# Kernel optimization log

Hardware: AMD Instinct MI355X
Metric: run time of the kernel (lower is better)

Reference implementation:

```python
import jax, jax.numpy as jnp
import numpy as np

H = 4096
N_HEADS = 32
N_KV = 8
HEAD_DIM = H // N_HEADS  # 128
GROUPS = N_HEADS // N_KV  # 4
FFN = 11008
EPS = 1e-5
B = 16
S_CACHE = 4096


def _rms(x, w):
    var = jnp.mean(x * x, axis=-1, keepdims=True)
    return w * (x * jax.lax.rsqrt(var + EPS))


def setup_inputs() -> dict:
    key = jax.random.key(0)
    ks = jax.random.split(key, 12)
    s = 0.02
    return {
        "hidden_states": jax.random.normal(ks[0], (B, 1, H), jnp.float32),
        "k_cache": jax.random.normal(ks[1], (B, N_KV, S_CACHE, HEAD_DIM), jnp.float32),
        "v_cache": jax.random.normal(ks[2], (B, N_KV, S_CACHE, HEAD_DIM), jnp.float32),
        "Wq": jax.random.normal(ks[3], (N_HEADS * HEAD_DIM, H), jnp.float32) * s,
        "Wk": jax.random.normal(ks[4], (N_KV * HEAD_DIM, H), jnp.float32) * s,
        "Wv": jax.random.normal(ks[5], (N_KV * HEAD_DIM, H), jnp.float32) * s,
        "Wo": jax.random.normal(ks[6], (H, N_HEADS * HEAD_DIM), jnp.float32) * s,
        "Wg": jax.random.normal(ks[7], (FFN, H), jnp.float32) * s,
        "Wu": jax.random.normal(ks[8], (FFN, H), jnp.float32) * s,
        "Wd": jax.random.normal(ks[9], (H, FFN), jnp.float32) * s,
        "ln1_w": jnp.ones((H,), jnp.float32),
        "ln2_w": jnp.ones((H,), jnp.float32),
    }


def reference(hidden_states, k_cache, v_cache, Wq, Wk, Wv, Wo, Wg, Wu, Wd, ln1_w, ln2_w):
    b = hidden_states.shape[0]
    residual = hidden_states
    h = _rms(hidden_states, ln1_w)  # [B,1,H]

    q = (h @ Wq.T).reshape(b, N_KV, GROUPS, HEAD_DIM)       # [B,kvH,G,D]
    k_new = (h @ Wk.T).reshape(b, N_KV, 1, HEAD_DIM)         # [B,kvH,1,D]
    v_new = (h @ Wv.T).reshape(b, N_KV, 1, HEAD_DIM)

    k = jnp.concatenate([k_cache, k_new], axis=2)            # [B,kvH,S+1,D]
    v = jnp.concatenate([v_cache, v_new], axis=2)

    scale = 1.0 / np.sqrt(HEAD_DIM)
    # GQA without materializing repeated KV heads (same math as repeat_interleave)
    scores = jnp.einsum("bkgd,bksd->bkgs", q, k) * scale      # [B,kvH,G,S+1]
    probs = jax.nn.softmax(scores.astype(jnp.float32), axis=-1).astype(q.dtype)
    attn = jnp.einsum("bkgs,bksd->bkgd", probs, v)            # [B,kvH,G,D]
    attn = attn.reshape(b, 1, N_HEADS * HEAD_DIM)

    h = residual + attn @ Wo.T                                # [B,1,H]

    residual = h
    h = _rms(h, ln2_w)
    mlp = (jax.nn.silu(h @ Wg.T) * (h @ Wu.T)) @ Wd.T
    return residual + mlp
```

## Files before the change

### kernel.cpp

```cpp
#include <hip/hip_runtime.h>
#include <math.h>

#define HH   4096
#define NKV  8
#define GRP  4
#define HD   128
#define FFN  11008
#define NB   16
#define SC   4096
#define SCALE 0.08838834764831845f
#define SCH  512
#define QKS  8

typedef float f4v __attribute__((ext_vector_type(4)));
typedef float f32x4 __attribute__((ext_vector_type(4)));
typedef short bf16x8 __attribute__((ext_vector_type(8)));
typedef unsigned short u16x4 __attribute__((ext_vector_type(4)));
typedef unsigned int u32x4v __attribute__((ext_vector_type(4)));

__device__ __forceinline__ f4v ntload4(const float* p) {
  return __builtin_nontemporal_load((const f4v*)p);
}
__device__ __forceinline__ float dot4(f4v a, f4v b) {
  return a[0] * b[0] + a[1] * b[1] + a[2] * b[2] + a[3] * b[3];
}
__device__ __forceinline__ unsigned short f2bf(float f) {
  unsigned int u = __builtin_bit_cast(unsigned int, f);
  u += 0x7fffu + ((u >> 16) & 1u);
  return (unsigned short)(u >> 16);
}
__device__ __forceinline__ float silu_f(float g) { return g / (1.f + __expf(-g)); }
__device__ __forceinline__ unsigned int cvtpk(float lo, float hi) {
  unsigned int r;
  asm("v_cvt_pk_bf16_f32 %0, %1, %2" : "=v"(r) : "v"(lo), "v"(hi));
  return r;
}

__global__ void rmsnorm_bf_k(const float* __restrict__ x, const float* __restrict__ w,
                             unsigned short* __restrict__ y) {
  int b = blockIdx.x;
  const float* xb = x + (size_t)b * HH;
  unsigned short* yb = y + (size_t)b * HH;
  int t = threadIdx.x, lane = t & 63, wave = t >> 6;
  f4v v[4];
  float ss = 0.f;
#pragma unroll
  for (int i = 0; i < 4; ++i) {
    v[i] = *(const f4v*)(xb + 4 * (t + 256 * i));
    ss += dot4(v[i], v[i]);
  }
#pragma unroll
  for (int m = 1; m < 64; m <<= 1) ss += __shfl_xor(ss, m);
  __shared__ float red[4];
  if (lane == 0) red[wave] = ss;
  __syncthreads();
  float tot = red[0] + red[1] + red[2] + red[3];
  float rs = rsqrtf(tot * (1.0f / HH) + 1e-5f);
#pragma unroll
  for (int i = 0; i < 4; ++i) {
    int h = 4 * (t + 256 * i);
    f4v wv = *(const f4v*)(w + h);
    f4v o = v[i] * rs * wv;
    u16x4 p;
#pragma unroll
    for (int j = 0; j < 4; ++j) p[j] = f2bf(o[j]);
    *(u16x4*)(yb + h) = p;
  }
}

template <int MODE>
__global__ __launch_bounds__(256, 4) void gemv_mfma_k(
    const float* __restrict__ W0, const float* __restrict__ W1,
    const float* __restrict__ W2, const unsigned short* __restrict__ xbf,
    float* __restrict__ part, int O, int H, int CH) {
  int t = threadIdx.x, lane = t & 63, wave = t >> 6;
  int rb = blockIdx.x, kc = blockIdx.y;
  int obase = rb * 64 + wave * 16;
  int orow = obase + (lane & 15);

  const float* Wp;
  if (MODE == 0) {
    if (orow < 4096) Wp = W0 + (size_t)orow * H;
    else if (orow < 5120) Wp = W1 + (size_t)(orow - 4096) * H;
    else Wp = W2 + (size_t)(orow - 5120) * H;
  } else if (MODE == 2) {
    Wp = (orow < FFN) ? W0 + (size_t)orow * H : W1 + (size_t)(orow - FFN) * H;
  } else {
    Wp = W0 + (size_t)orow * H;
  }

  int k0 = kc * CH + (lane >> 4) * 8;
  const float* wp = Wp + k0;
  const unsigned short* ap = xbf + (size_t)(lane & 15) * H + k0;

  f32x4 acc = {0.f, 0.f, 0.f, 0.f};
  int steps = CH / 32;
#pragma unroll 2
  for (int s = 0; s < steps; ++s) {
    f4v w0 = ntload4(wp);
    f4v w1 = ntload4(wp + 4);
    bf16x8 a = *(const bf16x8*)ap;
    bf16x8 bb;
#pragma unroll
    for (int j = 0; j < 4; ++j) {
      bb[j] = (short)f2bf(w0[j]);
      bb[4 + j] = (short)f2bf(w1[j]);
    }
    acc = __builtin_amdgcn_mfma_f32_16x16x32_bf16(a, bb, acc, 0, 0, 0);
    wp += 32;
    ap += 32;
  }
  float* pb = part + ((size_t)kc * NB + (size_t)((lane >> 4) * 4)) * O + orow;
#pragma unroll
  for (int r = 0; r < 4; ++r) pb[(size_t)r * O] = acc[r];
}

__global__ void rmsnorm2_k(const float* __restrict__ hid, const float* __restrict__ p1,
                           const float* __restrict__ w, float* __restrict__ h2,
                           unsigned short* __restrict__ xn2) {
  int b = blockIdx.x;
  int t = threadIdx.x, lane = t & 63, wave = t >> 6;
  f4v v[4];
  float ss = 0.f;
#pragma unroll
  for (int i = 0; i < 4; ++i) {
    int h = 4 * (t + 256 * i);
    f4v s = *(const f4v*)(hid + (size_t)b * HH + h);
#pragma unroll
    for (int ks = 0; ks < 8; ++ks)
      s += *(const f4v*)(p1 + ((size_t)(ks * NB + b)) * HH + h);
    v[i] = s;
    ss += dot4(s, s);
  }
#pragma unroll
  for (int m = 1; m < 64; m <<= 1) ss += __shfl_xor(ss, m);
  __shared__ float red[4];
  if (lane == 0) red[wave] = ss;
  __syncthreads();
  float tot = red[0] + red[1] + red[2] + red[3];
  float rs = rsqrtf(tot * (1.0f / HH) + 1e-5f);
#pragma unroll
  for (int i = 0; i < 4; ++i) {
    int h = 4 * (t + 256 * i);
    *(f4v*)(h2 + (size_t)b * HH + h) = v[i];
    f4v wv = *(const f4v*)(w + h);
    f4v o = v[i] * rs * wv;
    u16x4 p;
#pragma unroll
    for (int j = 0; j < 4; ++j) p[j] = f2bf(o[j]);
    *(u16x4*)(xn2 + (size_t)b * HH + h) = p;
  }
}

__global__ void red_gu_k(const float* __restrict__ p2, unsigned short* __restrict__ gu) {
  int idx = blockIdx.x * 256 + threadIdx.x;
  int pi = idx % 2752, b = idx / 2752;
  int p = pi * 4;
  const float* g0 = p2 + (size_t)b * 22016 + p;
  f4v g = *(const f4v*)g0 + *(const f4v*)(g0 + (size_t)NB * 22016);
  f4v u = *(const f4v*)(g0 + FFN) + *(const f4v*)(g0 + FFN + (size_t)NB * 22016);
  u16x4 pk;
#pragma unroll
  for (int j = 0; j < 4; ++j) pk[j] = f2bf(silu_f(g[j]) * u[j]);
  *(u16x4*)(gu + (size_t)b * FFN + p) = pk;
}

__global__ void red_out_k(const float* __restrict__ h2, const float* __restrict__ p3,
                          float* __restrict__ out) {
  int idx = blockIdx.x * 256 + threadIdx.x;
  int o = (idx & 1023) * 4, b = idx >> 10;
  f4v s = *(const f4v*)(h2 + (size_t)b * HH + o);
#pragma unroll
  for (int ks = 0; ks < 8; ++ks)
    s += *(const f4v*)(p3 + ((size_t)(ks * NB + b)) * HH + o);
  *(f4v*)(out + (size_t)b * HH + o) = s;
}

__global__ __launch_bounds__(256, 4) void attn_part_k(
    const float* __restrict__ pq, const float* __restrict__ kcache,
    const float* __restrict__ vcache, float* __restrict__ pm,
    float* __restrict__ pl, float* __restrict__ pacc) {
  int c = blockIdx.x, kv = blockIdx.y, b = blockIdx.z;
  int t = threadIdx.x, lane = t & 63, wave = t >> 6;
  int ds = lane & 15, ss = lane >> 4;
  __shared__ float qs[GRP * HD];
  __shared__ float sc[GRP][SCH];
  __shared__ float accw[4][GRP][HD];

  {
    int i0 = t * 2;
#pragma unroll
    for (int i = i0; i < i0 + 2; ++i) {
      int off = kv * (GRP * HD) + i;
      float s = 0.f;
#pragma unroll
      for (int kk = 0; kk < QKS; ++kk)
        s += pq[((size_t)kk * NB + b) * 6144 + off];
      qs[i] = s;
    }
  }
  __syncthreads();

  bf16x8 bq[4];
#pragma unroll
  for (int kk = 0; kk < 4; ++kk) {
    u32x4v w;
#pragma unroll
    for (int jj = 0; jj < 4; ++jj) {
      float f0 = 0.f, f1 = 0.f;
      if (ds < GRP) {
        int d = kk * 32 + ss * 8 + jj * 2;
        f0 = qs[ds * HD + d];
        f1 = qs[ds * HD + d + 1];
      }
      w[jj] = cvtpk(f0, f1);
    }
    bq[kk] = __builtin_bit_cast(bf16x8, w);
  }

  const size_t kvoff = ((size_t)b * NKV + kv) * (size_t)SC * HD;
  const float* kb = kcache + kvoff;

  for (int st = 0; st < SCH / 64; ++st) {
    int prel = (st * 4 + wave) * 16;
    const float* kr = kb + (size_t)(c * SCH + prel + ds) * HD + ss * 8;
    f32x4 d4 = {0.f, 0.f, 0.f, 0.f};
#pragma unroll
    for (int kk = 0; kk < 4; ++kk) {
      f4v k0 = *(const f4v*)(kr + kk * 32);
      f4v k1 = *(const f4v*)(kr + kk * 32 + 4);
      u32x4v w;
      w[0] = cvtpk(k0[0], k0[1]);
      w[1] = cvtpk(k0[2], k0[3]);
      w[2] = cvtpk(k1[0], k1[1]);
      w[3] = cvtpk(k1[2], k1[3]);
      d4 = __builtin_amdgcn_mfma_f32_16x16x32_bf16(
          __builtin_bit_cast(bf16x8, w), bq[kk], d4, 0, 0, 0);
    }
    if (ds < GRP) {
#pragma unroll
      for (int r = 0; r < 4; ++r) sc[ds][prel + ss * 4 + r] = d4[r] * SCALE;
    }
  }
  __syncthreads();

  size_t pbase = (((size_t)(b * NKV + kv)) * 8 + c) * GRP;
  {
    int g = wave;
    float m = -1e30f;
    for (int i = lane; i < SCH; i += 64) m = fmaxf(m, sc[g][i]);
#pragma unroll
    for (int mm = 1; mm < 64; mm <<= 1) m = fmaxf(m, __shfl_xor(m, mm));
    float lsum = 0.f;
    for (int i = lane; i < SCH; i += 64) {
      float e = __expf(sc[g][i] - m);
      sc[g][i] = e;
      lsum += e;
    }
#pragma unroll
    for (int mm = 1; mm < 64; mm <<= 1) lsum += __shfl_xor(lsum, mm);
    if (lane == 0) { pm[pbase + g] = m; pl[pbase + g] = lsum; }
  }
  __syncthreads();

  float acc[GRP][8];
#pragma unroll
  for (int g = 0; g < GRP; ++g)
#pragma unroll
    for (int j = 0; j < 8; ++j) acc[g][j] = 0.f;
  const float* vb = vcache + kvoff;
  for (int st = 0; st < SCH / 16; ++st) {
    int sl = st * 16 + wave * 4 + ss;
    const float* vr = vb + (size_t)(c * SCH + sl) * HD + 8 * ds;
    f4v v0 = ntload4(vr);
    f4v v1 = ntload4(vr + 4);
    float p[GRP];
#pragma unroll
    for (int g = 0; g < GRP; ++g) p[g] = sc[g][sl];
#pragma unroll
    for (int g = 0; g < GRP; ++g) {
#pragma unroll
      for (int j = 0; j < 4; ++j) {
        acc[g][j] += p[g] * v0[j];
        acc[g][4 + j] += p[g] * v1[j];
      }
    }
  }
#pragma unroll
  for (int m = 16; m < 64; m <<= 1)
#pragma unroll
    for (int g = 0; g < GRP; ++g)
#pragma unroll
      for (int j = 0; j < 8; ++j) acc[g][j] += __shfl_xor(acc[g][j], m);
  if (ss == 0) {
#pragma unroll
    for (int g = 0; g < GRP; ++g)
#pragma unroll
      for (int j = 0; j < 4; ++j) {
        accw[wave][g][8 * ds + j] = acc[g][j];
        accw[wave][g][8 * ds + 4 + j] = acc[g][4 + j];
      }
  }
  __syncthreads();

  for (int idx = t; idx < GRP * HD; idx += 256) {
    int g = idx >> 7, dd = idx & 127;
    float o = accw[0][g][dd] + accw[1][g][dd] + accw[2][g][dd] + accw[3][g][dd];
    pacc[(pbase + g) * HD + dd] = o;
  }
}

__global__ void attn_red_k(const float* __restrict__ pq, const float* __restrict__ pm,
                           const float* __restrict__ pl, const float* __restrict__ pacc,
                           unsigned short* __restrict__ attnb) {
  int bi = blockIdx.x;
  int b = bi >> 3, kv = bi & 7;
  int t = threadIdx.x, lane = t & 63, wave = t >> 6;
  __shared__ float sn[GRP];
  {
    int g = wave;
    int qoff = kv * (GRP * HD) + g * HD + 2 * lane;
    int koff = 4096 + kv * HD + 2 * lane;
    float qx = 0.f, qy = 0.f, kx = 0.f, ky = 0.f;
#pragma unroll
    for (int kk = 0; kk < QKS; ++kk) {
      const float* pp = pq + ((size_t)kk * NB + b) * 6144;
      qx += pp[qoff]; qy += pp[qoff + 1];
      kx += pp[koff]; ky += pp[koff + 1];
    }
    float d = qx * kx + qy * ky;
#pragma unroll
    for (int m = 1; m < 64; m <<= 1) d += __shfl_xor(d, m);
    if (lane == 0) sn[g] = d * SCALE;
  }
  __syncthreads();
  size_t base = ((size_t)(b * NKV + kv)) * 8;
  for (int idx = t; idx < GRP * HD; idx += 256) {
    int g = idx >> 7, dd = idx & 127;
    float snv = sn[g];
    float M = snv;
    float pmv[8];
#pragma unroll
    for (int cc = 0; cc < 8; ++cc) {
      pmv[cc] = pm[(base + cc) * GRP + g];
      M = fmaxf(M, pmv[cc]);
    }
    float vnv = 0.f;
#pragma unroll
    for (int kk = 0; kk < QKS; ++kk)
      vnv += pq[((size_t)kk * NB + b) * 6144 + 5120 + kv * HD + dd];
    float en = __expf(snv - M);
    float L = en;
    float o = en * vnv;
#pragma unroll
    for (int cc = 0; cc < 8; ++cc) {
      float f = __expf(pmv[cc] - M);
      L += f * pl[(base + cc) * GRP + g];
      o += f * pacc[((base + cc) * GRP + g) * HD + dd];
    }
    attnb[(size_t)b * HH + (size_t)(kv * GRP + g) * HD + dd] = f2bf(o / L);
  }
}

extern "C" void kernel_launch(void* const* d_in, const int* in_sizes, int n_in,
                              void* d_out, int out_size, void* d_ws, size_t ws_size,
                              hipStream_t stream) {
  const float* hidden = (const float*)d_in[0];
  const float* kc = (const float*)d_in[1];
  const float* vc = (const float*)d_in[2];
  const float* Wq = (const float*)d_in[3];
  const float* Wk = (const float*)d_in[4];
  const float* Wv = (const float*)d_in[5];
  const float* Wo = (const float*)d_in[6];
  const float* Wg = (const float*)d_in[7];
  const float* Wu = (const float*)d_in[8];
  const float* Wd = (const float*)d_in[9];
  const float* ln1 = (const float*)d_in[10];
  const float* ln2 = (const float*)d_in[11];
  float* out = (float*)d_out;

  float* p = (float*)d_ws;
  unsigned short* xn1bf = (unsigned short*)p;  p += 32768;
  unsigned short* attnbf = (unsigned short*)p; p += 32768;
  float* h2 = p;    p += 65536;
  unsigned short* xn2bf = (unsigned short*)p;  p += 32768;
  unsigned short* gubf = (unsigned short*)p;   p += 88064;
  float* pm = p;    p += 4096;
  float* pl = p;    p += 4096;
  float* pacc = p;  p += 524288;
  float* pq = p;    p += 786432;
  float* p1 = p;    p += 524288;
  float* p2 = pq;
  float* p3 = pacc;

  rmsnorm_bf_k<<<16, 256, 0, stream>>>(hidden, ln1, xn1bf);
  gemv_mfma_k<0><<<dim3(96, QKS), 256, 0, stream>>>(Wq, Wk, Wv, xn1bf, pq, 6144, 4096, 512);
  attn_part_k<<<dim3(8, 8, 16), 256, 0, stream>>>(pq, kc, vc, pm, pl, pacc);
  attn_red_k<<<128, 256, 0, stream>>>(pq, pm, pl, pacc, attnbf);
  gemv_mfma_k<1><<<dim3(64, 8), 256, 0, stream>>>(Wo, nullptr, nullptr, attnbf, p1, 4096, 4096, 512);
  rmsnorm2_k<<<16, 256, 0, stream>>>(hidden, p1, ln2, h2, xn2bf);
  gemv_mfma_k<2><<<dim3(344, 2), 256, 0, stream>>>(Wg, Wu, nullptr, xn2bf, p2, 22016, 4096, 2048);
  red_gu_k<<<172, 256, 0, stream>>>(p2, gubf);
  gemv_mfma_k<3><<<dim3(64, 8), 256, 0, stream>>>(Wd, nullptr, nullptr, gubf, p3, 4096, 11008, 1376);
  red_out_k<<<64, 256, 0, stream>>>(h2, p3, out);
}
```

Measured before the change: 286.9 us.

## Stage activations in LDS for MFMA GEMVs and widen blocks to 512 threads

The MFMA GEMV kernel now copies the block's bf16 activation slice into shared memory once and reads the MFMA A operand from LDS instead of global memory. Blocks grow to 8 waves covering 128 output rows, and the chunk size becomes a template parameter so loops are compile-time and unrolled by 4. The gate/up GEMV uses 4 K-splits instead of 2 and writes to dedicated partial buffers, so the reduction kernel sums 4 partials. This adds a sync and LDS footprint per block and changes the occupancy balance.

```diff
diff --git a/kernel.cpp b/kernel.cpp
--- a/kernel.cpp
+++ b/kernel.cpp
@@ -16,6 +16,7 @@
 typedef float f32x4 __attribute__((ext_vector_type(4)));
 typedef short bf16x8 __attribute__((ext_vector_type(8)));
 typedef unsigned short u16x4 __attribute__((ext_vector_type(4)));
+typedef unsigned short u16x8 __attribute__((ext_vector_type(8)));
 typedef unsigned int u32x4v __attribute__((ext_vector_type(4)));
 
 __device__ __forceinline__ f4v ntload4(const float* p) {
@@ -68,15 +69,15 @@
   }
 }
 
-template <int MODE>
-__global__ __launch_bounds__(256, 4) void gemv_mfma_k(
+template <int MODE, int KS, int CHT>
+__global__ __launch_bounds__(512, 4) void gemv_mfma_k(
     const float* __restrict__ W0, const float* __restrict__ W1,
     const float* __restrict__ W2, const unsigned short* __restrict__ xbf,
-    float* __restrict__ part, int O, int H, int CH) {
+    float* __restrict__ part, int O, int H) {
+  __shared__ unsigned short xs[NB][CHT + 8];
   int t = threadIdx.x, lane = t & 63, wave = t >> 6;
   int rb = blockIdx.x, kc = blockIdx.y;
-  int obase = rb * 64 + wave * 16;
-  int orow = obase + (lane & 15);
+  int orow = rb * 128 + wave * 16 + (lane & 15);
 
   const float* Wp;
   if (MODE == 0) {
@@ -89,17 +90,26 @@
     Wp = W0 + (size_t)orow * H;
   }
 
-  int k0 = kc * CH + (lane >> 4) * 8;
-  const float* wp = Wp + k0;
-  const unsigned short* ap = xbf + (size_t)(lane & 15) * H + k0;
+  {
+    constexpr int CPR = CHT / 8;
+    for (int c = t; c < NB * CPR; c += 512) {
+      int b = c / CPR, off = (c % CPR) * 8;
+      *(u16x8*)&xs[b][off] =
+          *(const u16x8*)(xbf + (size_t)b * H + (size_t)kc * CHT + off);
+    }
+  }
+  __syncthreads();
+
+  const unsigned short* xrow = &xs[lane & 15][(lane >> 4) * 8];
+  const float* wp = Wp + (size_t)kc * CHT + (lane >> 4) * 8;
 
   f32x4 acc = {0.f, 0.f, 0.f, 0.f};
-  int steps = CH / 32;
-#pragma unroll 2
+  constexpr int steps = CHT / 32;
+#pragma unroll 4
   for (int s = 0; s < steps; ++s) {
     f4v w0 = ntload4(wp);
     f4v w1 = ntload4(wp + 4);
-    bf16x8 a = *(const bf16x8*)ap;
+    bf16x8 a = *(const bf16x8*)(xrow + s * 32);
     bf16x8 bb;
 #pragma unroll
     for (int j = 0; j < 4; ++j) {
@@ -108,7 +118,6 @@
     }
     acc = __builtin_amdgcn_mfma_f32_16x16x32_bf16(a, bb, acc, 0, 0, 0);
     wp += 32;
-    ap += 32;
   }
   float* pb = part + ((size_t)kc * NB + (size_t)((lane >> 4) * 4)) * O + orow;
 #pragma unroll
@@ -156,9 +165,13 @@
   int idx = blockIdx.x * 256 + threadIdx.x;
   int pi = idx % 2752, b = idx / 2752;
   int p = pi * 4;
-  const float* g0 = p2 + (size_t)b * 22016 + p;
-  f4v g = *(const f4v*)g0 + *(const f4v*)(g0 + (size_t)NB * 22016);
-  f4v u = *(const f4v*)(g0 + FFN) + *(const f4v*)(g0 + FFN + (size_t)NB * 22016);
+  f4v g = {0.f, 0.f, 0.f, 0.f}, u = {0.f, 0.f, 0.f, 0.f};
+#pragma unroll
+  for (int kk = 0; kk < 4; ++kk) {
+    const float* base = p2 + ((size_t)(kk * NB + b)) * 22016;
+    g += *(const f4v*)(base + p);
+    u += *(const f4v*)(base + FFN + p);
+  }
   u16x4 pk;
 #pragma unroll
   for (int j = 0; j < 4; ++j) pk[j] = f2bf(silu_f(g[j]) * u[j]);
@@ -390,17 +403,17 @@
   float* pacc = p;  p += 524288;
   float* pq = p;    p += 786432;
   float* p1 = p;    p += 524288;
-  float* p2 = pq;
-  float* p3 = pacc;
+  float* p2 = p;    p += 1409024;
+  float* p3 = p;    p += 524288;
 
   rmsnorm_bf_k<<<16, 256, 0, stream>>>(hidden, ln1, xn1bf);
-  gemv_mfma_k<0><<<dim3(96, QKS), 256, 0, stream>>>(Wq, Wk, Wv, xn1bf, pq, 6144, 4096, 512);
+  gemv_mfma_k<0, QKS, 512><<<dim3(48, QKS), 512, 0, stream>>>(Wq, Wk, Wv, xn1bf, pq, 6144, 4096);
   attn_part_k<<<dim3(8, 8, 16), 256, 0, stream>>>(pq, kc, vc, pm, pl, pacc);
   attn_red_k<<<128, 256, 0, stream>>>(pq, pm, pl, pacc, attnbf);
-  gemv_mfma_k<1><<<dim3(64, 8), 256, 0, stream>>>(Wo, nullptr, nullptr, attnbf, p1, 4096, 4096, 512);
+  gemv_mfma_k<1, 8, 512><<<dim3(32, 8), 512, 0, stream>>>(Wo, nullptr, nullptr, attnbf, p1, 4096, 4096);
   rmsnorm2_k<<<16, 256, 0, stream>>>(hidden, p1, ln2, h2, xn2bf);
-  gemv_mfma_k<2><<<dim3(344, 2), 256, 0, stream>>>(Wg, Wu, nullptr, xn2bf, p2, 22016, 4096, 2048);
+  gemv_mfma_k<2, 4, 1024><<<dim3(172, 4), 512, 0, stream>>>(Wg, Wu, nullptr, xn2bf, p2, 22016, 4096);
   red_gu_k<<<172, 256, 0, stream>>>(p2, gubf);
-  gemv_mfma_k<3><<<dim3(64, 8), 256, 0, stream>>>(Wd, nullptr, nullptr, gubf, p3, 4096, 11008, 1376);
+  gemv_mfma_k<3, 8, 1376><<<dim3(32, 8), 512, 0, stream>>>(Wd, nullptr, nullptr, gubf, p3, 4096, 11008);
   red_out_k<<<64, 256, 0, stream>>>(h2, p3, out);
 }
```

After: 268.9 us. -6.3%, faster.
